# Kernel optimization log

Hardware: AMD Instinct MI355X
Metric: run time of the kernel (lower is better)

Reference implementation:

```python
import jax, jax.numpy as jnp
import numpy as np

B, T, C, H = 8, 1024, 768, 12
D = C // H  # head_dim = 64


def setup_inputs() -> dict:
    key = jax.random.key(0)
    ks = jax.random.split(key, 6)
    s = 1.0 / np.sqrt(C)
    x = jax.random.normal(ks[0], (B, T, C), dtype=jnp.float32)
    Wq = jax.random.normal(ks[1], (C, C), dtype=jnp.float32) * s
    Wk = jax.random.normal(ks[2], (C, C), dtype=jnp.float32) * s
    Wv = jax.random.normal(ks[3], (C, C), dtype=jnp.float32) * s
    Wo = jax.random.normal(ks[4], (C, C), dtype=jnp.float32) * s
    bq = jnp.zeros((C,), jnp.float32)
    bk = jnp.zeros((C,), jnp.float32)
    bv = jnp.zeros((C,), jnp.float32)
    bo = jnp.zeros((C,), jnp.float32)
    # causal mask, broadcastable to [B, H, T, T]
    mask = jnp.tril(jnp.ones((T, T), dtype=bool))[None, None, :, :]
    return {"x": x, "mask": mask, "Wq": Wq, "bq": bq, "Wk": Wk, "bk": bk,
            "Wv": Wv, "bv": bv, "Wo": Wo, "bo": bo}


def reference(x, mask, Wq, bq, Wk, bk, Wv, bv, Wo, bo):
    # QKV projections: [B,T,C] @ [C,C] -> [B,T,C]
    q = x @ Wq + bq
    k = x @ Wk + bk
    v = x @ Wv + bv
    # split heads -> [B,H,T,D]
    q = q.reshape(B, T, H, D).transpose(0, 2, 1, 3)
    k = k.reshape(B, T, H, D).transpose(0, 2, 1, 3)
    v = v.reshape(B, T, H, D).transpose(0, 2, 1, 3)
    scale = 1.0 / jnp.sqrt(jnp.float32(D))
    scores = jnp.einsum('bhtd,bhsd->bhts', q, k) * scale  # [B,H,T,T]
    scores = jnp.where(mask, scores, jnp.float32(-1e9))
    attn = jax.nn.softmax(scores, axis=-1)
    out = jnp.einsum('bhts,bhsd->bhtd', attn, v)  # [B,H,T,D]
    out = out.transpose(0, 2, 1, 3).reshape(B, T, C)
    return out @ Wo + bo
```

## Files before the change

### kernel.cpp

```cpp
#include <hip/hip_runtime.h>
#include <hip/hip_bf16.h>

#define B 8
#define T 1024
#define C 768
#define H 12
#define D 64
#define M (B * T)

typedef unsigned short u16;
typedef unsigned int u32;
typedef __attribute__((ext_vector_type(8))) short bf16x8;
typedef __attribute__((ext_vector_type(4))) float f32x4;

__device__ __forceinline__ u16 f2bf(float f) {
  union { float f; u32 u; } c; c.f = f;
  u32 r = c.u + 0x7FFF + ((c.u >> 16) & 1);
  return (u16)(r >> 16);
}

__device__ __forceinline__ void gload16(const void* g, void* l) {
  __builtin_amdgcn_global_load_lds(
      (const __attribute__((address_space(1))) void*)g,
      (__attribute__((address_space(3))) void*)l, 16, 0, 0);
}

__device__ __forceinline__ int swzA(int row) {
  return (row & 3) ^ ((row >> 2) & 1);
}

__global__ __launch_bounds__(256) void xconv_kernel(const float* __restrict__ in,
                                                    u16* __restrict__ out, int n4) {
  int i = blockIdx.x * 256 + threadIdx.x;
  int stride = gridDim.x * 256;
  for (; i < n4; i += stride) {
    float4 v = ((const float4*)in)[i];
    ushort4 o;
    o.x = f2bf(v.x); o.y = f2bf(v.y); o.z = f2bf(v.z); o.w = f2bf(v.w);
    ((ushort4*)out)[i] = o;
  }
}

__global__ __launch_bounds__(256) void wtrans_kernel(const float* __restrict__ Wq,
                                                     const float* __restrict__ Wk,
                                                     const float* __restrict__ Wv,
                                                     const float* __restrict__ Wo,
                                                     u16* __restrict__ WtQKV,
                                                     u16* __restrict__ WoT) {
  __shared__ float t[32][33];
  const int z = blockIdx.z;
  const float* W = (z == 0) ? Wq : (z == 1) ? Wk : (z == 2) ? Wv : Wo;
  u16* dst = (z < 3) ? (WtQKV + (size_t)z * 768 * 768) : WoT;
  const int k0 = blockIdx.y * 32, n0 = blockIdx.x * 32;
  const int tx = threadIdx.x & 31, ty = threadIdx.x >> 5;
#pragma unroll
  for (int i = 0; i < 4; i++) {
    int r = ty * 4 + i;
    t[r][tx] = W[(size_t)(k0 + r) * 768 + n0 + tx];
  }
  __syncthreads();
#pragma unroll
  for (int i = 0; i < 4; i++) {
    int r = ty * 4 + i;
    dst[(size_t)(n0 + r) * 768 + k0 + tx] = f2bf(t[tx][r]);
  }
}

template <typename OutT, bool ROWBIAS, int BN>
__global__ __launch_bounds__(256) void gemm_mfma_kernel(
    const u16* __restrict__ A,
    const u16* __restrict__ Wt,
    const float* __restrict__ b0, const float* __restrict__ b1,
    OutT* __restrict__ o0, OutT* __restrict__ o1,
    int ldOut, float sc0, float sc1) {
  constexpr int NJ = BN / 32;
  constexpr int BT = BN * 4 / 256;
  __shared__ u16 As[128 * 32];
  __shared__ u16 Bs[BN * 32];
  const int tid = threadIdx.x;
  const int w = tid >> 6, l = tid & 63;
  const int g = l >> 4, c = l & 15;
  const int m0 = blockIdx.y * 128;
  const int n0g = blockIdx.x * BN;
  const int seg = (!ROWBIAS && n0g >= 768) ? 1 : 0;
  const int n0 = n0g - seg * 768;
  const float* bias = (seg == 0) ? b0 : b1;
  OutT* out = (seg == 0) ? o0 : o1;
  const float sc = (seg == 0) ? sc0 : sc1;
  const int wr = (w >> 1) * 64, wc = (w & 1) * (BN / 2);

  f32x4 acc[4][NJ];
#pragma unroll
  for (int i = 0; i < 4; i++)
#pragma unroll
    for (int j = 0; j < NJ; j++) acc[i][j] = f32x4{0.f, 0.f, 0.f, 0.f};

  for (int k0 = 0; k0 < 768; k0 += 32) {
    __syncthreads();
#pragma unroll
    for (int t = 0; t < 2; t++) {
      int ii = w * 2 + t;
      int e16 = ii * 64 + l;
      int row = e16 >> 2, slot = e16 & 3;
      int gs = slot ^ swzA(row);
      gload16(A + (size_t)(m0 + row) * 768 + k0 + gs * 8, (char*)As + ii * 1024);
    }
#pragma unroll
    for (int t = 0; t < BT; t++) {
      int ii = w * BT + t;
      int e16 = ii * 64 + l;
      int row = e16 >> 2, slot = e16 & 3;
      int gs = slot ^ swzA(row);
      gload16(Wt + (size_t)(n0g + row) * 768 + k0 + gs * 8, (char*)Bs + ii * 1024);
    }
    __syncthreads();

    bf16x8 af[4], bfr[NJ];
#pragma unroll
    for (int i = 0; i < 4; i++) {
      int row = wr + i * 16 + c;
      int slot = g ^ swzA(row);
      af[i] = *(const bf16x8*)(As + row * 32 + slot * 8);
    }
#pragma unroll
    for (int j = 0; j < NJ; j++) {
      int row = wc + j * 16 + c;
      int slot = g ^ swzA(row);
      bfr[j] = *(const bf16x8*)(Bs + row * 32 + slot * 8);
    }
#pragma unroll
    for (int i = 0; i < 4; i++)
#pragma unroll
      for (int j = 0; j < NJ; j++)
        acc[i][j] = __builtin_amdgcn_mfma_f32_16x16x32_bf16(af[i], bfr[j], acc[i][j], 0, 0, 0);
  }

  float brow[4][4];
  if (ROWBIAS) {
#pragma unroll
    for (int i = 0; i < 4; i++)
#pragma unroll
      for (int r = 0; r < 4; r++)
        brow[i][r] = b0[m0 + wr + i * 16 + g * 4 + r];
  }
#pragma unroll
  for (int j = 0; j < NJ; j++) {
    int col = n0 + wc + j * 16 + c;
    float bcol = ROWBIAS ? 0.f : bias[col];
#pragma unroll
    for (int i = 0; i < 4; i++) {
#pragma unroll
      for (int r = 0; r < 4; r++) {
        int row = m0 + wr + i * 16 + g * 4 + r;
        float v = (acc[i][j][r] + (ROWBIAS ? brow[i][r] : bcol)) * sc;
        if constexpr (sizeof(OutT) == 2) {
          ((u16*)out)[(size_t)row * ldOut + col] = f2bf(v);
        } else {
          ((float*)out)[(size_t)row * ldOut + col] = v;
        }
      }
    }
  }
}

__global__ __launch_bounds__(256) void attn_mfma_kernel(
    const u16* __restrict__ Qb, const u16* __restrict__ Kb,
    const u16* __restrict__ VT, u16* __restrict__ Ob) {
  __shared__ u16 Ks[128 * 64];
  __shared__ u16 Vs[64 * 128];
  __shared__ u16 Ps[4][16][132];

  const int tid = threadIdx.x;
  const int w = tid >> 6, l = tid & 63;
  const int g = l >> 4, c = l & 15;

  const int wg = blockIdx.x;
  const int logical = (wg & 7) * 192 + (wg >> 3);
  const int bh = logical >> 4;
  const int qi = 15 - (logical & 15);
  const int q0 = qi * 64;
  const int b = bh / H, h = bh % H;
  const int qw = q0 + w * 16;

  bf16x8 qf[2];
  {
    size_t base = (size_t)(b * T + qw + c) * C + h * D;
    qf[0] = *(const bf16x8*)(Qb + base + g * 8);
    qf[1] = *(const bf16x8*)(Qb + base + 32 + g * 8);
  }

  f32x4 acc[4];
#pragma unroll
  for (int j = 0; j < 4; j++) acc[j] = f32x4{0.f, 0.f, 0.f, 0.f};
  float m_i[4], l_p[4];
#pragma unroll
  for (int r = 0; r < 4; r++) { m_i[r] = -1e30f; l_p[r] = 0.f; }

  const int nt = q0 / 128 + 1;
  for (int it = 0; it < nt; it++) {
    const int s0 = it * 128;
    __syncthreads();
#pragma unroll
    for (int t = 0; t < 4; t++) {
      int ii = w * 4 + t;
      int e16 = ii * 64 + l;
      int row = e16 >> 3, slot = e16 & 7;
      int gs = slot ^ (row & 7);
      gload16(Kb + (size_t)(b * T + s0 + row) * C + h * D + gs * 8, (char*)Ks + ii * 1024);
    }
#pragma unroll
    for (int t = 0; t < 4; t++) {
      int ii = w * 4 + t;
      int e16 = ii * 64 + l;
      int row = e16 >> 4, slot = e16 & 15;
      int gs = slot ^ (row & 15);
      gload16(VT + (size_t)(h * D + row) * M + b * T + s0 + gs * 8, (char*)Vs + ii * 1024);
    }
    __syncthreads();

    const bool active = (s0 <= qw + 15);
    if (active) {
      f32x4 s[8];
#pragma unroll
      for (int f = 0; f < 8; f++) s[f] = f32x4{0.f, 0.f, 0.f, 0.f};
#pragma unroll
      for (int f = 0; f < 8; f++) {
        int kvrow = f * 16 + c;
#pragma unroll
        for (int kc = 0; kc < 2; kc++) {
          int slot = (kc * 4 + g) ^ (kvrow & 7);
          bf16x8 kf = *(const bf16x8*)(Ks + kvrow * 64 + slot * 8);
          s[f] = __builtin_amdgcn_mfma_f32_16x16x32_bf16(qf[kc], kf, s[f], 0, 0, 0);
        }
      }
      const bool partial = (s0 + 127 > qw);
      if (partial) {
#pragma unroll
        for (int r = 0; r < 4; r++) {
          int q = qw + g * 4 + r;
#pragma unroll
          for (int f = 0; f < 8; f++) {
            int kv = s0 + f * 16 + c;
            if (kv > q) s[f][r] = -1e30f;
          }
        }
      }
      float mx[4];
#pragma unroll
      for (int r = 0; r < 4; r++) {
        float mr = s[0][r];
#pragma unroll
        for (int f = 1; f < 8; f++) mr = fmaxf(mr, s[f][r]);
        mx[r] = mr;
      }
#pragma unroll
      for (int off = 1; off < 16; off <<= 1)
#pragma unroll
        for (int r = 0; r < 4; r++) mx[r] = fmaxf(mx[r], __shfl_xor(mx[r], off, 64));
      bool defer = true;
#pragma unroll
      for (int r = 0; r < 4; r++) defer = defer && (mx[r] <= m_i[r] + 8.0f);
      if (!__all(defer)) {
#pragma unroll
        for (int r = 0; r < 4; r++) {
          float mn = fmaxf(m_i[r], mx[r]);
          float rc = exp2f(m_i[r] - mn);
          m_i[r] = mn;
          l_p[r] *= rc;
#pragma unroll
          for (int j = 0; j < 4; j++) acc[j][r] *= rc;
        }
      }
#pragma unroll
      for (int r = 0; r < 4; r++) {
        float sum = 0.f;
#pragma unroll
        for (int f = 0; f < 8; f++) {
          float p = exp2f(s[f][r] - m_i[r]);
          s[f][r] = p;
          sum += p;
        }
        l_p[r] += sum;
#pragma unroll
        for (int f = 0; f < 8; f += 2) {
          __hip_bfloat162 h2 = __float22bfloat162_rn(make_float2(s[f][r], s[f + 1][r]));
          u32 pk = *(u32*)&h2;
          Ps[w][g * 4 + r][f * 16 + c] = (u16)pk;
          Ps[w][g * 4 + r][(f + 1) * 16 + c] = (u16)(pk >> 16);
        }
      }
#pragma unroll
      for (int kc = 0; kc < 4; kc++) {
        bf16x8 pf = *(const bf16x8*)(&Ps[w][c][kc * 32 + g * 8]);
#pragma unroll
        for (int j = 0; j < 4; j++) {
          bf16x8 vf = *(const bf16x8*)(Vs + (j * 16 + c) * 128 + (((kc * 4 + g) ^ c) * 8));
          acc[j] = __builtin_amdgcn_mfma_f32_16x16x32_bf16(pf, vf, acc[j], 0, 0, 0);
        }
      }
    }
  }

  float inv[4];
#pragma unroll
  for (int r = 0; r < 4; r++) {
    float v = l_p[r];
#pragma unroll
    for (int off = 1; off < 16; off <<= 1) v += __shfl_xor(v, off, 64);
    inv[r] = 1.f / v;
  }
#pragma unroll
  for (int j = 0; j < 4; j++) {
#pragma unroll
    for (int r = 0; r < 4; r++) {
      int row = qw + g * 4 + r;
      int col = j * 16 + c;
      Ob[(size_t)(b * T + row) * C + h * D + col] = f2bf(acc[j][r] * inv[r]);
    }
  }
}

extern "C" void kernel_launch(void* const* d_in, const int* in_sizes, int n_in,
                              void* d_out, int out_size, void* d_ws, size_t ws_size,
                              hipStream_t stream) {
  const float* x  = (const float*)d_in[0];
  const float* Wq = (const float*)d_in[2];
  const float* bq = (const float*)d_in[3];
  const float* Wk = (const float*)d_in[4];
  const float* bk = (const float*)d_in[5];
  const float* Wv = (const float*)d_in[6];
  const float* bv = (const float*)d_in[7];
  const float* Wo = (const float*)d_in[8];
  const float* bo = (const float*)d_in[9];
  float* out = (float*)d_out;

  const size_t MC2 = (size_t)M * C * 2;
  char* ws = (char*)d_ws;
  u16* xb    = (u16*)(ws);
  u16* WtQKV = (u16*)(ws + MC2);
  u16* WoT   = (u16*)(ws + MC2 + 3538944);
  u16* Qb    = (u16*)(ws + MC2 + 3538944 + 1179648);
  u16* Kb    = (u16*)((char*)Qb + MC2);
  u16* VT    = (u16*)((char*)Kb + MC2);
  u16* Ob    = (u16*)((char*)VT + MC2);
  u16* WvT   = WtQKV + 2 * 768 * 768;

  const float qscale = 0.125f * 1.4426950408889634f;

  xconv_kernel<<<2048, 256, 0, stream>>>(x, xb, M * C / 4);
  wtrans_kernel<<<dim3(24, 24, 4), 256, 0, stream>>>(Wq, Wk, Wv, Wo, WtQKV, WoT);
  gemm_mfma_kernel<u16, false, 128><<<dim3(12, 64), 256, 0, stream>>>(
      xb, WtQKV, bq, bk, Qb, Kb, 768, qscale, 1.f);
  gemm_mfma_kernel<u16, true, 64><<<dim3(128, 6), 256, 0, stream>>>(
      WvT, xb, bv, bv, VT, VT, M, 1.f, 1.f);
  attn_mfma_kernel<<<1536, 256, 0, stream>>>(Qb, Kb, VT, Ob);
  gemm_mfma_kernel<float, false, 64><<<dim3(12, 64), 256, 0, stream>>>(
      Ob, WoT, bo, bo, out, out, 768, 1.f, 1.f);
}
```

Measured before the change: 140.0 us.

## Merge prep kernels, add MFMA priority hints, and widen GEMM tiles

Fuses the x bf16 conversion and weight transpose into one prep kernel launch with a flattened grid, removing a launch and the gap between the two. Wraps the attention MFMA loops in s_setprio raises so waves issuing matrix ops get scheduling priority over softmax/load waves. Switches the V-projection and output GEMMs from BN=64 to BN=128 tiles, halving their block counts for more reuse per block at the cost of fewer blocks and possibly lower occupancy.

```diff
diff --git a/kernel.cpp b/kernel.cpp
--- a/kernel.cpp
+++ b/kernel.cpp
@@ -29,39 +29,39 @@
   return (row & 3) ^ ((row >> 2) & 1);
 }
 
-__global__ __launch_bounds__(256) void xconv_kernel(const float* __restrict__ in,
-                                                    u16* __restrict__ out, int n4) {
-  int i = blockIdx.x * 256 + threadIdx.x;
-  int stride = gridDim.x * 256;
-  for (; i < n4; i += stride) {
-    float4 v = ((const float4*)in)[i];
-    ushort4 o;
-    o.x = f2bf(v.x); o.y = f2bf(v.y); o.z = f2bf(v.z); o.w = f2bf(v.w);
-    ((ushort4*)out)[i] = o;
-  }
-}
-
-__global__ __launch_bounds__(256) void wtrans_kernel(const float* __restrict__ Wq,
-                                                     const float* __restrict__ Wk,
-                                                     const float* __restrict__ Wv,
-                                                     const float* __restrict__ Wo,
-                                                     u16* __restrict__ WtQKV,
-                                                     u16* __restrict__ WoT) {
+__global__ __launch_bounds__(256) void prep_kernel(
+    const float* __restrict__ x,
+    const float* __restrict__ Wq, const float* __restrict__ Wk,
+    const float* __restrict__ Wv, const float* __restrict__ Wo,
+    u16* __restrict__ xb, u16* __restrict__ WtQKV, u16* __restrict__ WoT) {
   __shared__ float t[32][33];
-  const int z = blockIdx.z;
+  const int bx = blockIdx.x;
+  if (bx < 2048) {
+    const int n4 = M * C / 4;
+    for (int i = bx * 256 + threadIdx.x; i < n4; i += 2048 * 256) {
+      float4 v = ((const float4*)x)[i];
+      ushort4 o;
+      o.x = f2bf(v.x); o.y = f2bf(v.y); o.z = f2bf(v.z); o.w = f2bf(v.w);
+      ((ushort4*)xb)[i] = o;
+    }
+    return;
+  }
+  const int i = bx - 2048;
+  const int z = i / 576;
+  const int rem = i % 576;
+  const int k0 = (rem / 24) * 32, n0 = (rem % 24) * 32;
   const float* W = (z == 0) ? Wq : (z == 1) ? Wk : (z == 2) ? Wv : Wo;
   u16* dst = (z < 3) ? (WtQKV + (size_t)z * 768 * 768) : WoT;
-  const int k0 = blockIdx.y * 32, n0 = blockIdx.x * 32;
   const int tx = threadIdx.x & 31, ty = threadIdx.x >> 5;
 #pragma unroll
-  for (int i = 0; i < 4; i++) {
-    int r = ty * 4 + i;
+  for (int j = 0; j < 4; j++) {
+    int r = ty * 4 + j;
     t[r][tx] = W[(size_t)(k0 + r) * 768 + n0 + tx];
   }
   __syncthreads();
 #pragma unroll
-  for (int i = 0; i < 4; i++) {
-    int r = ty * 4 + i;
+  for (int j = 0; j < 4; j++) {
+    int r = ty * 4 + j;
     dst[(size_t)(n0 + r) * 768 + k0 + tx] = f2bf(t[tx][r]);
   }
 }
@@ -223,6 +223,7 @@
       f32x4 s[8];
 #pragma unroll
       for (int f = 0; f < 8; f++) s[f] = f32x4{0.f, 0.f, 0.f, 0.f};
+      __builtin_amdgcn_s_setprio(1);
 #pragma unroll
       for (int f = 0; f < 8; f++) {
         int kvrow = f * 16 + c;
@@ -233,6 +234,7 @@
           s[f] = __builtin_amdgcn_mfma_f32_16x16x32_bf16(qf[kc], kf, s[f], 0, 0, 0);
         }
       }
+      __builtin_amdgcn_s_setprio(0);
       const bool partial = (s0 + 127 > qw);
       if (partial) {
 #pragma unroll
@@ -289,6 +291,7 @@
           Ps[w][g * 4 + r][(f + 1) * 16 + c] = (u16)(pk >> 16);
         }
       }
+      __builtin_amdgcn_s_setprio(1);
 #pragma unroll
       for (int kc = 0; kc < 4; kc++) {
         bf16x8 pf = *(const bf16x8*)(&Ps[w][c][kc * 32 + g * 8]);
@@ -298,6 +301,7 @@
           acc[j] = __builtin_amdgcn_mfma_f32_16x16x32_bf16(pf, vf, acc[j], 0, 0, 0);
         }
       }
+      __builtin_amdgcn_s_setprio(0);
     }
   }
 
@@ -347,13 +351,12 @@
 
   const float qscale = 0.125f * 1.4426950408889634f;
 
-  xconv_kernel<<<2048, 256, 0, stream>>>(x, xb, M * C / 4);
-  wtrans_kernel<<<dim3(24, 24, 4), 256, 0, stream>>>(Wq, Wk, Wv, Wo, WtQKV, WoT);
+  prep_kernel<<<4352, 256, 0, stream>>>(x, Wq, Wk, Wv, Wo, xb, WtQKV, WoT);
   gemm_mfma_kernel<u16, false, 128><<<dim3(12, 64), 256, 0, stream>>>(
       xb, WtQKV, bq, bk, Qb, Kb, 768, qscale, 1.f);
-  gemm_mfma_kernel<u16, true, 64><<<dim3(128, 6), 256, 0, stream>>>(
+  gemm_mfma_kernel<u16, true, 128><<<dim3(64, 6), 256, 0, stream>>>(
       WvT, xb, bv, bv, VT, VT, M, 1.f, 1.f);
   attn_mfma_kernel<<<1536, 256, 0, stream>>>(Qb, Kb, VT, Ob);
-  gemm_mfma_kernel<float, false, 64><<<dim3(12, 64), 256, 0, stream>>>(
+  gemm_mfma_kernel<float, false, 128><<<dim3(6, 64), 256, 0, stream>>>(
       Ob, WoT, bo, bo, out, out, 768, 1.f, 1.f);
 }
```

New measurement: 137.1 us. -2.1%, faster.
